# Kernel optimization log

Hardware: AMD Instinct MI355X
Metric: run time of the kernel (lower is better)

The kernel has to match this reference:

```python
import jax, jax.numpy as jnp
import numpy as np

B, N, P = 16, 128, 4096          # images, proposals/img, pairs/img
D_IN, D_HID = 1024, 512          # input_dim, hidden_dim
D_GEO, D_EMB = 128, 200          # geometry_feat_dim, embed_dim
N_OBJ, N_REL = 151, 51           # obj classes, rel classes (out_dim = 50)
OUT = N_REL - 1
LN_EPS = 1e-5


def _ln(x, g, b):
    mu = jnp.mean(x, axis=-1, keepdims=True)
    var = jnp.var(x, axis=-1, keepdims=True)
    return (x - mu) * jax.lax.rsqrt(var + LN_EPS) * g + b


def setup_inputs() -> dict:
    key = jax.random.key(0)
    ks = jax.random.split(key, 20)
    w = lambda k, shape: (jax.random.normal(k, shape, jnp.float32) * 0.02)
    return {
        'visual_feat': jax.random.normal(ks[0], (B * P, D_IN), jnp.float32),
        'box_info': jax.random.uniform(ks[1], (B, N, 9), jnp.float32),
        'pred_logits': jax.random.normal(ks[2], (B, N, N_OBJ), jnp.float32),
        'pair_idx': jax.random.randint(ks[3], (B, P, 2), 0, N, jnp.int32),
        'obj_sem_w': w(ks[4], (N_OBJ, D_EMB)),
        'pos_w1': w(ks[5], (9, D_GEO)), 'pos_b1': jnp.zeros((D_GEO,), jnp.float32),
        'pos_w2': w(ks[6], (D_GEO, D_GEO)), 'pos_b2': jnp.zeros((D_GEO,), jnp.float32),
        'vis_w': w(ks[7], (D_IN, D_HID)), 'vis_b': jnp.zeros((D_HID,), jnp.float32),
        'geo_w': w(ks[8], (2 * D_EMB + 2 * D_GEO, D_HID)), 'geo_b': jnp.zeros((D_HID,), jnp.float32),
        'fus_g': jnp.ones((2 * D_HID,), jnp.float32), 'fus_bt': jnp.zeros((2 * D_HID,), jnp.float32),
        'fus_w': w(ks[9], (2 * D_HID, D_HID)), 'fus_b': jnp.zeros((D_HID,), jnp.float32),
        'cls_g': jnp.ones((D_HID,), jnp.float32), 'cls_bt': jnp.zeros((D_HID,), jnp.float32),
        'cls_w': w(ks[10], (D_HID, OUT)), 'cls_b': jnp.zeros((OUT,), jnp.float32),
    }


def reference(visual_feat, box_info, pred_logits, pair_idx,
              obj_sem_w, pos_w1, pos_b1, pos_w2, pos_b2,
              vis_w, vis_b, geo_w, geo_b,
              fus_g, fus_bt, fus_w, fus_b,
              cls_g, cls_bt, cls_w, cls_b):
    # detach() in torch -> stop_gradient
    vf = jax.lax.stop_gradient(visual_feat)
    pl = jax.lax.stop_gradient(pred_logits)
    # vis_embed = Sequential(ReLU, Linear): [B*P, D_IN] -> [B, P, D_HID]
    vis = (jnp.maximum(vf, 0.0) @ vis_w + vis_b).reshape(B, P, D_HID)
    # obj_pos_embed = Linear, ReLU, Linear: [B, N, 9] -> [B, N, D_GEO]
    pos = jnp.maximum(box_info @ pos_w1 + pos_b1, 0.0) @ pos_w2 + pos_b2
    # semantic embed: softmax over obj classes @ embedding table -> [B, N, D_EMB]
    sem = jax.nn.softmax(pl, axis=-1) @ obj_sem_w
    bidx = jnp.arange(B)[:, None]
    s, o = pair_idx[..., 0], pair_idx[..., 1]
    # gather pair reps: [B, P, 2*(D_GEO+D_EMB)]
    rep = jnp.concatenate([pos[bidx, s], sem[bidx, s], pos[bidx, o], sem[bidx, o]], axis=-1)
    # proposal_box_feat_extract = Sequential(ReLU, Linear)
    geo = jnp.maximum(rep, 0.0) @ geo_w + geo_b
    # proposal_feat_fusion = Sequential(LayerNorm, ReLU, Linear)
    fused = jnp.concatenate([vis, geo], axis=-1)
    fused = jnp.maximum(_ln(fused, fus_g, fus_bt), 0.0) @ fus_w + fus_b
    # proposal_relness_cls_fc = Sequential(LayerNorm, ReLU, Linear)
    logits = jnp.maximum(_ln(fused, cls_g, cls_bt), 0.0) @ cls_w + cls_b  # [B, P, OUT]
    # predictor_type == 'single': scatter max sigmoid score into NxN matrix
    scores = jnp.max(jax.nn.sigmoid(logits), axis=-1)  # [B, P]
    rel_mat = jnp.zeros((B, N, N), logits.dtype).at[bidx, s, o].set(scores)
    return logits.reshape(B * P, OUT), rel_mat
```

## Files before the change

kernel.cpp:

```cpp
#include <hip/hip_runtime.h>
#include <cstdint>

#define B_    16
#define N_    128
#define P_    4096
#define M_    65536
#define DIN   1024
#define DHID  512
#define DGEO  128
#define DEMB  200
#define NODEF 328
#define NOBJ  151
#define OUTC  50
#define KGEO  656
#define KGEOP 672

typedef __attribute__((ext_vector_type(8))) short bf16x8;
typedef __attribute__((ext_vector_type(4))) float f32x4;

typedef __attribute__((address_space(3))) unsigned char lds_u8;
typedef __attribute__((address_space(1))) unsigned char glb_u8;

static __device__ __forceinline__ void async_copy16(const void* g, void* l) {
  __builtin_amdgcn_global_load_lds((const glb_u8*)g, (lds_u8*)l, 16, 0, 0);
}

static __device__ __forceinline__ unsigned short f2b(float f) {
  union { float f; unsigned u; } v; v.f = f;
  unsigned r = v.u + 0x7fffu + ((v.u >> 16) & 1u);
  return (unsigned short)(r >> 16);
}
static __device__ __forceinline__ float b2f(unsigned short b) {
  union { unsigned u; float f; } v; v.u = ((unsigned)b) << 16;
  return v.f;
}
static __device__ __forceinline__ unsigned pack2(float a, float b) {
  return (unsigned)f2b(a) | ((unsigned)f2b(b) << 16);
}
static __device__ __forceinline__ void unpack8(uint4 raw, float* x) {
  x[0] = b2f(raw.x & 0xffffu); x[1] = b2f(raw.x >> 16);
  x[2] = b2f(raw.y & 0xffffu); x[3] = b2f(raw.y >> 16);
  x[4] = b2f(raw.z & 0xffffu); x[5] = b2f(raw.z >> 16);
  x[6] = b2f(raw.w & 0xffffu); x[7] = b2f(raw.w >> 16);
}

#define ZN   131072
#define TV   (512 * 1024)
#define TG   (512 * KGEOP)
#define TF   (512 * 1024)
#define TC   (128 * 512)
#define PREP_TOT (ZN + TV + TG + TF + TC)
__global__ __launch_bounds__(256)
void prep_kernel(uint4* __restrict__ scat,
                 const float* __restrict__ vis_w, unsigned short* __restrict__ wT_vis,
                 const float* __restrict__ geo_w, unsigned short* __restrict__ wT_geo,
                 const float* __restrict__ fus_w, unsigned short* __restrict__ wT_fus,
                 const float* __restrict__ cls_w, unsigned short* __restrict__ wT_cls) {
  int idx = blockIdx.x * 256 + threadIdx.x;
  if (idx < ZN) { scat[idx] = make_uint4(0, 0, 0, 0); return; }
  idx -= ZN;
  if (idx < TV) {
    int n = idx >> 10, k = idx & 1023;
    wT_vis[idx] = f2b(vis_w[(size_t)k * 512 + n]);
    return;
  }
  idx -= TV;
  if (idx < TG) {
    int n = idx / KGEOP, k = idx - n * KGEOP;
    wT_geo[idx] = (k < KGEO) ? f2b(geo_w[(size_t)k * 512 + n]) : 0;
    return;
  }
  idx -= TG;
  if (idx < TF) {
    int n = idx >> 10, k = idx & 1023;
    wT_fus[idx] = f2b(fus_w[(size_t)k * 512 + n]);
    return;
  }
  idx -= TF;
  if (idx < TC) {
    int n = idx >> 9, k = idx & 511;
    wT_cls[idx] = (n < OUTC) ? f2b(cls_w[(size_t)k * OUTC + n]) : 0;
  }
}

__global__ __launch_bounds__(128)
void node_kernel(const float* __restrict__ box, const float* __restrict__ plog,
                 const float* __restrict__ semw,
                 const float* __restrict__ w1, const float* __restrict__ b1,
                 const float* __restrict__ w2, const float* __restrict__ b2,
                 unsigned short* __restrict__ nodeFb) {
  const int node = blockIdx.x;
  const int t = threadIdx.x;
  __shared__ float sBox[9];
  __shared__ float sH[128];
  __shared__ float sE[NOBJ];
  __shared__ float sRed[4];
  if (t < 9) sBox[t] = box[node * 9 + t];
  float l0 = (t < NOBJ) ? plog[node * NOBJ + t] : -1e30f;
  float l1 = (t + 128 < NOBJ) ? plog[node * NOBJ + t + 128] : -1e30f;
  __syncthreads();
  float h = b1[t];
#pragma unroll
  for (int i = 0; i < 9; i++) h = fmaf(sBox[i], w1[i * 128 + t], h);
  h = fmaxf(h, 0.f);
  sH[t] = h;
  float mx = fmaxf(l0, l1);
#pragma unroll
  for (int off = 32; off >= 1; off >>= 1) mx = fmaxf(mx, __shfl_xor(mx, off));
  if ((t & 63) == 0) sRed[t >> 6] = mx;
  __syncthreads();
  mx = fmaxf(sRed[0], sRed[1]);
  float e0 = (t < NOBJ) ? expf(l0 - mx) : 0.f;
  float e1 = (t + 128 < NOBJ) ? expf(l1 - mx) : 0.f;
  if (t < NOBJ) sE[t] = e0;
  if (t + 128 < NOBJ) sE[t + 128] = e1;
  float sm = e0 + e1;
#pragma unroll
  for (int off = 32; off >= 1; off >>= 1) sm += __shfl_xor(sm, off);
  if ((t & 63) == 0) sRed[2 + (t >> 6)] = sm;
  __syncthreads();
  const float inv = 1.f / (sRed[2] + sRed[3]);
  float pv = b2[t];
  for (int i = 0; i < 128; i++) pv = fmaf(sH[i], w2[i * 128 + t], pv);
  nodeFb[(size_t)node * NODEF + t] = f2b(fmaxf(pv, 0.f));
  float a0 = 0.f, a1 = 0.f;
  const int d1 = (t + 128 < DEMB) ? (t + 128) : 0;
  for (int i = 0; i < NOBJ; i++) {
    float e = sE[i];
    a0 = fmaf(e, semw[i * DEMB + t], a0);
    a1 = fmaf(e, semw[i * DEMB + d1], a1);
  }
  nodeFb[(size_t)node * NODEF + 128 + t] = f2b(fmaxf(a0 * inv, 0.f));
  if (t + 128 < DEMB) nodeFb[(size_t)node * NODEF + 128 + t + 128] = f2b(fmaxf(a1 * inv, 0.f));
}

template<int D>
__global__ __launch_bounds__(256)
void ln_relu_kernel(unsigned short* __restrict__ X,
                    const float* __restrict__ g, const float* __restrict__ bta) {
  constexpr int C = D / 64;
  const int lane = threadIdx.x & 63, wv = threadIdx.x >> 6;
  const size_t row = (size_t)blockIdx.x * 4 + wv;
  unsigned short* xp = X + row * D + lane * C;
  float x[C];
#pragma unroll
  for (int c = 0; c < C; c += 8) {
    uint4 raw = *(const uint4*)(xp + c);
    unpack8(raw, x + c);
  }
  float s = 0.f, s2 = 0.f;
#pragma unroll
  for (int q = 0; q < C; q++) { s += x[q]; s2 = fmaf(x[q], x[q], s2); }
#pragma unroll
  for (int off = 32; off >= 1; off >>= 1) { s += __shfl_xor(s, off); s2 += __shfl_xor(s2, off); }
  const float mu = s / D;
  const float rs = rsqrtf(s2 / D - mu * mu + 1e-5f);
  const float* gp = g + lane * C;
  const float* bp = bta + lane * C;
#pragma unroll
  for (int c = 0; c < C; c += 8) {
    float4 g0 = *(const float4*)(gp + c), g1 = *(const float4*)(gp + c + 4);
    float4 t0 = *(const float4*)(bp + c), t1 = *(const float4*)(bp + c + 4);
    float y0 = fmaxf(fmaf((x[c + 0] - mu) * rs, g0.x, t0.x), 0.f);
    float y1 = fmaxf(fmaf((x[c + 1] - mu) * rs, g0.y, t0.y), 0.f);
    float y2 = fmaxf(fmaf((x[c + 2] - mu) * rs, g0.z, t0.z), 0.f);
    float y3 = fmaxf(fmaf((x[c + 3] - mu) * rs, g0.w, t0.w), 0.f);
    float y4 = fmaxf(fmaf((x[c + 4] - mu) * rs, g1.x, t1.x), 0.f);
    float y5 = fmaxf(fmaf((x[c + 5] - mu) * rs, g1.y, t1.y), 0.f);
    float y6 = fmaxf(fmaf((x[c + 6] - mu) * rs, g1.z, t1.z), 0.f);
    float y7 = fmaxf(fmaf((x[c + 7] - mu) * rs, g1.w, t1.w), 0.f);
    uint4 u;
    u.x = pack2(y0, y1); u.y = pack2(y2, y3);
    u.z = pack2(y4, y5); u.w = pack2(y6, y7);
    *(uint4*)(xp + c) = u;
  }
}

template<int MODE>
__global__ __launch_bounds__(512, 4)
void gemmW(const void* __restrict__ Asrc, int ldaE,
           const unsigned short* __restrict__ Bt, int Ktot,
           const float* __restrict__ bias,
           unsigned short* __restrict__ C, int ldcE, int ccol0,
           const int* __restrict__ pidx,
           const unsigned short* __restrict__ nodeFb,
           const unsigned short* __restrict__ zsrc) {
  const int NS = Ktot >> 5;
  __shared__ __align__(16) unsigned char smem[8192 + 65536];
  const int tid = threadIdx.x, lane = tid & 63, w = tid >> 6;
  const int bm = blockIdx.x;

  const int ar = tid >> 3;
  const int ak = tid & 7;
  const int aswz = (ar & 3) ^ ((ar >> 2) & 3);
  unsigned char* aDst = smem + ar * 64 + (((ak >> 1) ^ aswz) << 4) + (ak & 1) * 8;

  const unsigned short* nbS = nullptr;
  const unsigned short* nbO = nullptr;
  const unsigned char* aG = nullptr;
  if (MODE == 2) {
    int pr = bm * 64 + ar;
    int2 so = *(const int2*)(pidx + 2 * pr);
    int b = pr >> 12;
    nbS = nodeFb + (size_t)((b << 7) + so.x) * NODEF;
    nbO = nodeFb + (size_t)((b << 7) + so.y) * NODEF;
  } else if (MODE == 1) {
    aG = (const unsigned char*)Asrc + (size_t)(bm * 64 + ar) * ldaE * 4 + ak * 16;
  } else {
    aG = (const unsigned char*)Asrc + (size_t)(bm * 64 + ar) * ldaE * 2 + ak * 8;
  }

  const int gsB = (lane & 3) ^ ((lane >> 2) & 3) ^ ((lane >> 4) & 3);
  int bOff[4];
#pragma unroll
  for (int i = 0; i < 4; i++) {
    int col = (w * 4 + i) * 16 + (lane >> 2);
    bOff[i] = col * Ktot * 2 + gsB * 16;
  }
  const unsigned char* bBase = (const unsigned char*)Bt;

  uint2 ra2[2]; uint4 ra4[2];
  auto issueA = [&](int s, int set) {
    if (MODE == 0) {
      ra2[set] = *(const uint2*)(aG + (size_t)s * 64);
    } else if (MODE == 1) {
      ra4[set] = *(const uint4*)(aG + (size_t)s * 128);
    } else {
      const int e0 = s * 32 + ak * 4;
      uintptr_t sel = (e0 < NODEF) ? (uintptr_t)(nbS + e0)
                    : (e0 < KGEO)  ? (uintptr_t)(nbO + (e0 - NODEF))
                                   : (uintptr_t)zsrc;
      ra2[set] = *(const uint2*)sel;
    }
  };
  auto issueB = [&](int s) {
    unsigned char* lb = smem + 8192 + (s & 1) * 32768 + w * 4096;
#pragma unroll
    for (int i = 0; i < 4; i++)
      async_copy16(bBase + (size_t)bOff[i] + (size_t)s * 64, lb + i * 1024);
  };
  auto writeA = [&](int s, int set) {
    uint2 d;
    if (MODE == 1) {
      float f0 = fmaxf(__uint_as_float(ra4[set].x), 0.f);
      float f1 = fmaxf(__uint_as_float(ra4[set].y), 0.f);
      float f2 = fmaxf(__uint_as_float(ra4[set].z), 0.f);
      float f3 = fmaxf(__uint_as_float(ra4[set].w), 0.f);
      d.x = pack2(f0, f1); d.y = pack2(f2, f3);
    } else d = ra2[set];
    *(uint2*)(aDst + (s & 1) * 4096) = d;
  };

  const int wm = w >> 2, wn = w & 3;
  const int frow = lane & 15;
  const int szf = (frow & 3) ^ ((frow >> 2) & 3);
  const int koff = (((lane >> 4) ^ szf) << 4);
  const int aRowB = (wm * 32 + frow) * 64;
  const int bColB = (wn * 128 + frow) * 64;

  f32x4 acc[2][8];
#pragma unroll
  for (int m = 0; m < 2; m++)
#pragma unroll
    for (int n = 0; n < 8; n++) acc[m][n] = (f32x4){0.f, 0.f, 0.f, 0.f};

  issueA(0, 0); issueB(0);
  issueA(1, 1); issueB(1);

#pragma unroll 1
  for (int s2 = 0; s2 < NS; s2 += 2) {
#pragma unroll
    for (int h = 0; h < 2; h++) {
      const int sc = s2 + h;
      if (sc >= NS) break;
      if (sc == NS - 1) asm volatile("s_waitcnt vmcnt(0)" ::: "memory");
      else              asm volatile("s_waitcnt vmcnt(5)" ::: "memory");
      __builtin_amdgcn_sched_barrier(0);
      writeA(sc, h);
      if (sc + 2 < NS) issueA(sc + 2, h);
      asm volatile("s_waitcnt lgkmcnt(0)" ::: "memory");
      __builtin_amdgcn_s_barrier();
      __builtin_amdgcn_sched_barrier(0);
      const unsigned char* ab = smem + (sc & 1) * 4096;
      const unsigned char* bb = smem + 8192 + (sc & 1) * 32768;
      bf16x8 af0 = *(const bf16x8*)(ab + aRowB + koff);
      bf16x8 af1 = *(const bf16x8*)(ab + aRowB + 16 * 64 + koff);
      __builtin_amdgcn_s_setprio(1);
#pragma unroll
      for (int n = 0; n < 8; n++) {
        bf16x8 bf = *(const bf16x8*)(bb + bColB + n * 16 * 64 + koff);
        acc[0][n] = __builtin_amdgcn_mfma_f32_16x16x32_bf16(af0, bf, acc[0][n], 0, 0, 0);
        acc[1][n] = __builtin_amdgcn_mfma_f32_16x16x32_bf16(af1, bf, acc[1][n], 0, 0, 0);
      }
      __builtin_amdgcn_s_setprio(0);
      __builtin_amdgcn_sched_barrier(0);
      __builtin_amdgcn_s_barrier();
      __builtin_amdgcn_sched_barrier(0);
      if (sc + 2 < NS) issueB(sc + 2);
    }
  }
  const int rb = bm * 64 + wm * 32 + ((lane >> 4) << 2);
  const int cb = wn * 128 + frow;
#pragma unroll
  for (int n = 0; n < 8; n++) {
    const int col = cb + n * 16;
    const float bv = bias[col];
#pragma unroll
    for (int m = 0; m < 2; m++)
#pragma unroll
      for (int i = 0; i < 4; i++) {
        const int row = rb + m * 16 + i;
        C[(size_t)row * ldcE + ccol0 + col] = f2b(acc[m][n][i] + bv);
      }
  }
}

__global__ __launch_bounds__(256)
void gemm_cls(const unsigned short* __restrict__ A, int lda,
              const unsigned short* __restrict__ Bt,
              const float* __restrict__ bias,
              float* __restrict__ C,
              int Ktot,
              const int* __restrict__ pidx,
              unsigned long long* __restrict__ scat) {
  __shared__ unsigned short ldsA[128 * 64];
  __shared__ unsigned short ldsB[128 * 64];
  const int tid = threadIdx.x;
  const int lane = tid & 63, wid = tid >> 6;
  const int cpx = gridDim.x >> 3;
  const int bm = (blockIdx.x & 7) * cpx + (blockIdx.x >> 3);

  const int srow = wid * 32 + (lane >> 3);
  const int skof = (lane & 7) * 8;
  const unsigned short* ag = A + (size_t)(bm * 128 + srow) * lda + skof;
  const unsigned short* bg = Bt + (size_t)srow * Ktot + skof;

  f32x4 acc[4][4];
#pragma unroll
  for (int m = 0; m < 4; m++)
#pragma unroll
    for (int n = 0; n < 4; n++) acc[m][n] = (f32x4){0.f, 0.f, 0.f, 0.f};

  const int wm = wid >> 1, wn = wid & 1;
  const int frow = lane & 15;
  const int kgrp = (lane >> 4) << 3;

  for (int kt = 0; kt < Ktot; kt += 64) {
#pragma unroll
    for (int i = 0; i < 4; i++) {
      async_copy16(ag + (size_t)i * 8 * lda + kt, &ldsA[wid * 2048 + i * 512]);
      async_copy16(bg + (size_t)i * 8 * Ktot + kt, &ldsB[wid * 2048 + i * 512]);
    }
    __syncthreads();
#pragma unroll
    for (int kk = 0; kk < 64; kk += 32) {
      bf16x8 af[4], bfr[4];
#pragma unroll
      for (int m = 0; m < 4; m++)
        af[m] = *(const bf16x8*)&ldsA[(wm * 64 + m * 16 + frow) * 64 + kk + kgrp];
#pragma unroll
      for (int n = 0; n < 4; n++)
        bfr[n] = *(const bf16x8*)&ldsB[(wn * 64 + n * 16 + frow) * 64 + kk + kgrp];
#pragma unroll
      for (int m = 0; m < 4; m++)
#pragma unroll
        for (int n = 0; n < 4; n++)
          acc[m][n] = __builtin_amdgcn_mfma_f32_16x16x32_bf16(af[m], bfr[n], acc[m][n], 0, 0, 0);
    }
    __syncthreads();
  }
  const int rb = bm * 128 + wm * 64 + ((lane >> 4) << 2);
#pragma unroll
  for (int n = 0; n < 4; n++) {
    const int col = wn * 64 + frow + n * 16;
    const float bv = (col < OUTC) ? bias[col] : 0.f;
#pragma unroll
    for (int m = 0; m < 4; m++)
#pragma unroll
      for (int i = 0; i < 4; i++) {
        const int row = rb + m * 16 + i;
        if (col < OUTC) C[(size_t)row * OUTC + col] = acc[m][n][i] + bv;
      }
  }
  if (wn == 0) {
#pragma unroll
    for (int m = 0; m < 4; m++)
#pragma unroll
      for (int i = 0; i < 4; i++) {
        float mx = -1e30f;
#pragma unroll
        for (int n = 0; n < 4; n++) {
          const int col = n * 16 + frow;
          float v = acc[m][n][i] + ((col < OUTC) ? bias[col] : 0.f);
          if (col < OUTC) mx = fmaxf(mx, v);
        }
        mx = fmaxf(mx, __shfl_xor(mx, 1));
        mx = fmaxf(mx, __shfl_xor(mx, 2));
        mx = fmaxf(mx, __shfl_xor(mx, 4));
        mx = fmaxf(mx, __shfl_xor(mx, 8));
        if (frow == 0) {
          const int row = rb + m * 16 + i;
          float sc = 1.f / (1.f + expf(-mx));
          int b = row >> 12, p = row & 4095;
          int s = pidx[2 * row], o = pidx[2 * row + 1];
          unsigned long long key = (((unsigned long long)(p + 1)) << 32) |
                                   (unsigned long long)__float_as_uint(sc);
          atomicMax(&scat[((size_t)(b * N_ + s) << 7) + o], key);
        }
      }
  }
}

__global__ void relmat_kernel(const unsigned long long* __restrict__ scat, float* __restrict__ out) {
  int i = blockIdx.x * blockDim.x + threadIdx.x;
  if (i >= B_ * N_ * N_) return;
  unsigned long long v = scat[i];
  out[i] = v ? __uint_as_float((unsigned)(v & 0xffffffffu)) : 0.f;
}

extern "C" void kernel_launch(void* const* d_in, const int* in_sizes, int n_in,
                              void* d_out, int out_size, void* d_ws, size_t ws_size,
                              hipStream_t stream) {
  const float* visual_feat = (const float*)d_in[0];
  const float* box_info    = (const float*)d_in[1];
  const float* pred_logits = (const float*)d_in[2];
  const int*   pair_idx    = (const int*)d_in[3];
  const float* obj_sem_w   = (const float*)d_in[4];
  const float* pos_w1 = (const float*)d_in[5];
  const float* pos_b1 = (const float*)d_in[6];
  const float* pos_w2 = (const float*)d_in[7];
  const float* pos_b2 = (const float*)d_in[8];
  const float* vis_w  = (const float*)d_in[9];
  const float* vis_b  = (const float*)d_in[10];
  const float* geo_w  = (const float*)d_in[11];
  const float* geo_b  = (const float*)d_in[12];
  const float* fus_g  = (const float*)d_in[13];
  const float* fus_bt = (const float*)d_in[14];
  const float* fus_w  = (const float*)d_in[15];
  const float* fus_b  = (const float*)d_in[16];
  const float* cls_g  = (const float*)d_in[17];
  const float* cls_bt = (const float*)d_in[18];
  const float* cls_w  = (const float*)d_in[19];
  const float* cls_b  = (const float*)d_in[20];

  char* ws = (char*)d_ws;
  size_t off = 0;
  auto alloc = [&](size_t bytes) { char* p = ws + off; off += (bytes + 255) & ~(size_t)255; return p; };
  unsigned short* fused  = (unsigned short*)alloc((size_t)M_ * 1024 * 2);
  unsigned short* fused2 = (unsigned short*)alloc((size_t)M_ * 512 * 2);
  unsigned short* nodeFb = (unsigned short*)alloc((size_t)B_ * N_ * NODEF * 2);
  unsigned short* wT_vis = (unsigned short*)alloc((size_t)512 * 1024 * 2);
  unsigned short* wT_geo = (unsigned short*)alloc((size_t)512 * KGEOP * 2);
  unsigned short* wT_fus = (unsigned short*)alloc((size_t)512 * 1024 * 2);
  unsigned short* wT_cls = (unsigned short*)alloc((size_t)128 * 512 * 2);
  unsigned long long* scat = (unsigned long long*)alloc((size_t)B_ * N_ * N_ * 8);

  float* out_logits = (float*)d_out;
  float* out_rel = out_logits + (size_t)M_ * OUTC;

  prep_kernel<<<dim3((PREP_TOT + 255) / 256), 256, 0, stream>>>(
      (uint4*)scat, vis_w, wT_vis, geo_w, wT_geo, fus_w, wT_fus, cls_w, wT_cls);
  node_kernel<<<dim3(B_ * N_), 128, 0, stream>>>(box_info, pred_logits, obj_sem_w,
                                                 pos_w1, pos_b1, pos_w2, pos_b2, nodeFb);
  gemmW<2><<<dim3(M_ / 64), 512, 0, stream>>>(nullptr, 0, wT_geo, KGEOP, geo_b,
                                              fused, 1024, 512,
                                              pair_idx, nodeFb, (const unsigned short*)scat);
  gemmW<1><<<dim3(M_ / 64), 512, 0, stream>>>(visual_feat, 1024, wT_vis, 1024, vis_b,
                                              fused, 1024, 0,
                                              nullptr, nullptr, nullptr);
  ln_relu_kernel<1024><<<dim3(M_ / 4), 256, 0, stream>>>(fused, fus_g, fus_bt);
  gemmW<0><<<dim3(M_ / 64), 512, 0, stream>>>(fused, 1024, wT_fus, 1024, fus_b,
                                              fused2, 512, 0,
                                              nullptr, nullptr, nullptr);
  ln_relu_kernel<512><<<dim3(M_ / 4), 256, 0, stream>>>(fused2, cls_g, cls_bt);
  gemm_cls<<<dim3(512), 256, 0, stream>>>(fused2, 512, wT_cls, cls_b,
                                          out_logits, 512, pair_idx, scat);
  relmat_kernel<<<dim3((B_ * N_ * N_) / 256), 256, 0, stream>>>(scat, out_rel);
}
```

Before: 464.7 us.

## Stage GEMM A tiles via async LDS copies with 4-deep pipeline; prepass relu-cast vis input

The GEMM kernel now loads its A operand with direct global-to-LDS async copies issued by half the waves into a 4-stage ring buffer, instead of loading through registers and writing LDS by hand. The LDS swizzle changes to match. Because the fp32 visual features cannot be relu'd and cast in flight anymore, a separate relu+bf16 cast kernel writes a bf16 copy into a reused workspace buffer before the visual GEMM. This is meant to deepen prefetch and cut register traffic and VALU work in the GEMM main loop. The cost is an extra full pass over the 256 MB fp32 input plus a 128 MB bf16 write, and more LDS per block.

```diff
diff --git a/kernel.cpp b/kernel.cpp
--- a/kernel.cpp
+++ b/kernel.cpp
@@ -134,6 +134,20 @@
   if (t + 128 < DEMB) nodeFb[(size_t)node * NODEF + 128 + t + 128] = f2b(fmaxf(a1 * inv, 0.f));
 }
 
+__global__ __launch_bounds__(256)
+void relu_cast_kernel(const float* __restrict__ in, unsigned short* __restrict__ out, int n8) {
+  for (int i = blockIdx.x * blockDim.x + threadIdx.x; i < n8; i += gridDim.x * blockDim.x) {
+    float4 v0 = ((const float4*)in)[2 * i];
+    float4 v1 = ((const float4*)in)[2 * i + 1];
+    uint4 u;
+    u.x = pack2(fmaxf(v0.x, 0.f), fmaxf(v0.y, 0.f));
+    u.y = pack2(fmaxf(v0.z, 0.f), fmaxf(v0.w, 0.f));
+    u.z = pack2(fmaxf(v1.x, 0.f), fmaxf(v1.y, 0.f));
+    u.w = pack2(fmaxf(v1.z, 0.f), fmaxf(v1.w, 0.f));
+    ((uint4*)out)[i] = u;
+  }
+}
+
 template<int D>
 __global__ __launch_bounds__(256)
 void ln_relu_kernel(unsigned short* __restrict__ X,
@@ -178,83 +192,69 @@
 
 template<int MODE>
 __global__ __launch_bounds__(512, 4)
-void gemmW(const void* __restrict__ Asrc, int ldaE,
-           const unsigned short* __restrict__ Bt, int Ktot,
-           const float* __restrict__ bias,
-           unsigned short* __restrict__ C, int ldcE, int ccol0,
-           const int* __restrict__ pidx,
-           const unsigned short* __restrict__ nodeFb,
-           const unsigned short* __restrict__ zsrc) {
+void gemmW2(const unsigned short* __restrict__ A, int ldaE,
+            const unsigned short* __restrict__ Bt, int Ktot,
+            const float* __restrict__ bias,
+            unsigned short* __restrict__ C, int ldcE, int ccol0,
+            const int* __restrict__ pidx,
+            const unsigned short* __restrict__ nodeFb,
+            const unsigned short* __restrict__ zsrc) {
   const int NS = Ktot >> 5;
-  __shared__ __align__(16) unsigned char smem[8192 + 65536];
+  __shared__ __align__(16) unsigned char smem[16384 + 65536];
   const int tid = threadIdx.x, lane = tid & 63, w = tid >> 6;
   const int bm = blockIdx.x;
 
-  const int ar = tid >> 3;
-  const int ak = tid & 7;
-  const int aswz = (ar & 3) ^ ((ar >> 2) & 3);
-  unsigned char* aDst = smem + ar * 64 + (((ak >> 1) ^ aswz) << 4) + (ak & 1) * 8;
-
+  const unsigned short* aS = nullptr;
   const unsigned short* nbS = nullptr;
   const unsigned short* nbO = nullptr;
-  const unsigned char* aG = nullptr;
-  if (MODE == 2) {
-    int pr = bm * 64 + ar;
-    int2 so = *(const int2*)(pidx + 2 * pr);
-    int b = pr >> 12;
-    nbS = nodeFb + (size_t)((b << 7) + so.x) * NODEF;
-    nbO = nodeFb + (size_t)((b << 7) + so.y) * NODEF;
-  } else if (MODE == 1) {
-    aG = (const unsigned char*)Asrc + (size_t)(bm * 64 + ar) * ldaE * 4 + ak * 16;
-  } else {
-    aG = (const unsigned char*)Asrc + (size_t)(bm * 64 + ar) * ldaE * 2 + ak * 8;
-  }
-
-  const int gsB = (lane & 3) ^ ((lane >> 2) & 3) ^ ((lane >> 4) & 3);
+  int aslot8 = 0;
+  if (w < 4) {
+    const int arow = w * 16 + (lane >> 2);
+    const int aslot = (lane & 3) ^ ((lane >> 3) & 3);
+    aslot8 = aslot * 8;
+    if (MODE == 0) {
+      aS = A + (size_t)(bm * 64 + arow) * ldaE + aslot8;
+    } else {
+      int pr = bm * 64 + arow;
+      int2 so = *(const int2*)(pidx + 2 * pr);
+      int b = pr >> 12;
+      nbS = nodeFb + (size_t)((b << 7) + so.x) * NODEF;
+      nbO = nodeFb + (size_t)((b << 7) + so.y) * NODEF;
+    }
+  }
+  auto stageA = [&](int s) {
+    if (w < 4) {
+      unsigned char* la = smem + (s & 3) * 4096 + w * 1024;
+      if (MODE == 0) {
+        async_copy16(aS + (size_t)s * 32, la);
+      } else {
+        const int e = s * 32 + aslot8;
+        uintptr_t sel = (e < NODEF) ? (uintptr_t)(nbS + e)
+                      : (e < KGEO)  ? (uintptr_t)(nbO + (e - NODEF))
+                                    : (uintptr_t)zsrc;
+        async_copy16((const void*)sel, la);
+      }
+    }
+  };
+
+  const unsigned char* bBase = (const unsigned char*)Bt;
+  const int gsB = (lane & 3) ^ ((lane >> 3) & 3);
   int bOff[4];
 #pragma unroll
   for (int i = 0; i < 4; i++) {
     int col = (w * 4 + i) * 16 + (lane >> 2);
     bOff[i] = col * Ktot * 2 + gsB * 16;
   }
-  const unsigned char* bBase = (const unsigned char*)Bt;
-
-  uint2 ra2[2]; uint4 ra4[2];
-  auto issueA = [&](int s, int set) {
-    if (MODE == 0) {
-      ra2[set] = *(const uint2*)(aG + (size_t)s * 64);
-    } else if (MODE == 1) {
-      ra4[set] = *(const uint4*)(aG + (size_t)s * 128);
-    } else {
-      const int e0 = s * 32 + ak * 4;
-      uintptr_t sel = (e0 < NODEF) ? (uintptr_t)(nbS + e0)
-                    : (e0 < KGEO)  ? (uintptr_t)(nbO + (e0 - NODEF))
-                                   : (uintptr_t)zsrc;
-      ra2[set] = *(const uint2*)sel;
-    }
-  };
-  auto issueB = [&](int s) {
-    unsigned char* lb = smem + 8192 + (s & 1) * 32768 + w * 4096;
+  auto stageB = [&](int s) {
+    unsigned char* lb = smem + 16384 + (s & 1) * 32768 + w * 4096;
 #pragma unroll
     for (int i = 0; i < 4; i++)
       async_copy16(bBase + (size_t)bOff[i] + (size_t)s * 64, lb + i * 1024);
   };
-  auto writeA = [&](int s, int set) {
-    uint2 d;
-    if (MODE == 1) {
-      float f0 = fmaxf(__uint_as_float(ra4[set].x), 0.f);
-      float f1 = fmaxf(__uint_as_float(ra4[set].y), 0.f);
-      float f2 = fmaxf(__uint_as_float(ra4[set].z), 0.f);
-      float f3 = fmaxf(__uint_as_float(ra4[set].w), 0.f);
-      d.x = pack2(f0, f1); d.y = pack2(f2, f3);
-    } else d = ra2[set];
-    *(uint2*)(aDst + (s & 1) * 4096) = d;
-  };
 
   const int wm = w >> 2, wn = w & 3;
   const int frow = lane & 15;
-  const int szf = (frow & 3) ^ ((frow >> 2) & 3);
-  const int koff = (((lane >> 4) ^ szf) << 4);
+  const int koff = (((lane >> 4) ^ ((frow >> 1) & 3)) << 4);
   const int aRowB = (wm * 32 + frow) * 64;
   const int bColB = (wn * 128 + frow) * 64;
 
@@ -264,40 +264,36 @@
 #pragma unroll
     for (int n = 0; n < 8; n++) acc[m][n] = (f32x4){0.f, 0.f, 0.f, 0.f};
 
-  issueA(0, 0); issueB(0);
-  issueA(1, 1); issueB(1);
+  stageA(0); stageA(1); stageA(2); stageA(3);
+  stageB(0); stageB(1);
 
 #pragma unroll 1
-  for (int s2 = 0; s2 < NS; s2 += 2) {
-#pragma unroll
-    for (int h = 0; h < 2; h++) {
-      const int sc = s2 + h;
-      if (sc >= NS) break;
-      if (sc == NS - 1) asm volatile("s_waitcnt vmcnt(0)" ::: "memory");
-      else              asm volatile("s_waitcnt vmcnt(5)" ::: "memory");
-      __builtin_amdgcn_sched_barrier(0);
-      writeA(sc, h);
-      if (sc + 2 < NS) issueA(sc + 2, h);
-      asm volatile("s_waitcnt lgkmcnt(0)" ::: "memory");
-      __builtin_amdgcn_s_barrier();
-      __builtin_amdgcn_sched_barrier(0);
-      const unsigned char* ab = smem + (sc & 1) * 4096;
-      const unsigned char* bb = smem + 8192 + (sc & 1) * 32768;
-      bf16x8 af0 = *(const bf16x8*)(ab + aRowB + koff);
-      bf16x8 af1 = *(const bf16x8*)(ab + aRowB + 16 * 64 + koff);
-      __builtin_amdgcn_s_setprio(1);
-#pragma unroll
-      for (int n = 0; n < 8; n++) {
-        bf16x8 bf = *(const bf16x8*)(bb + bColB + n * 16 * 64 + koff);
-        acc[0][n] = __builtin_amdgcn_mfma_f32_16x16x32_bf16(af0, bf, acc[0][n], 0, 0, 0);
-        acc[1][n] = __builtin_amdgcn_mfma_f32_16x16x32_bf16(af1, bf, acc[1][n], 0, 0, 0);
-      }
-      __builtin_amdgcn_s_setprio(0);
-      __builtin_amdgcn_sched_barrier(0);
-      __builtin_amdgcn_s_barrier();
-      __builtin_amdgcn_sched_barrier(0);
-      if (sc + 2 < NS) issueB(sc + 2);
+  for (int sc = 0; sc < NS; ++sc) {
+    if (sc == NS - 1)
+      asm volatile("s_waitcnt vmcnt(0)" ::: "memory");
+    else if (w >= 4 || sc == 0 || sc >= NS - 3)
+      asm volatile("s_waitcnt vmcnt(4)" ::: "memory");
+    else
+      asm volatile("s_waitcnt vmcnt(5)" ::: "memory");
+    __builtin_amdgcn_s_barrier();
+    __builtin_amdgcn_sched_barrier(0);
+    const unsigned char* ab = smem + (sc & 3) * 4096;
+    const unsigned char* bb = smem + 16384 + (sc & 1) * 32768;
+    bf16x8 af0 = *(const bf16x8*)(ab + aRowB + koff);
+    bf16x8 af1 = *(const bf16x8*)(ab + aRowB + 16 * 64 + koff);
+    __builtin_amdgcn_s_setprio(1);
+#pragma unroll
+    for (int n = 0; n < 8; n++) {
+      bf16x8 bf = *(const bf16x8*)(bb + bColB + n * 16 * 64 + koff);
+      acc[0][n] = __builtin_amdgcn_mfma_f32_16x16x32_bf16(af0, bf, acc[0][n], 0, 0, 0);
+      acc[1][n] = __builtin_amdgcn_mfma_f32_16x16x32_bf16(af1, bf, acc[1][n], 0, 0, 0);
     }
+    __builtin_amdgcn_s_setprio(0);
+    __builtin_amdgcn_sched_barrier(0);
+    __builtin_amdgcn_s_barrier();
+    __builtin_amdgcn_sched_barrier(0);
+    if (sc + 4 < NS) stageA(sc + 4);
+    if (sc + 2 < NS) stageB(sc + 2);
   }
   const int rb = bm * 64 + wm * 32 + ((lane >> 4) << 2);
   const int cb = wn * 128 + frow;
@@ -446,8 +442,8 @@
   char* ws = (char*)d_ws;
   size_t off = 0;
   auto alloc = [&](size_t bytes) { char* p = ws + off; off += (bytes + 255) & ~(size_t)255; return p; };
-  unsigned short* fused  = (unsigned short*)alloc((size_t)M_ * 1024 * 2);
-  unsigned short* fused2 = (unsigned short*)alloc((size_t)M_ * 512 * 2);
+  unsigned short* fused = (unsigned short*)alloc((size_t)M_ * 1024 * 2);
+  unsigned short* R1    = (unsigned short*)alloc((size_t)M_ * 1024 * 2);
   unsigned short* nodeFb = (unsigned short*)alloc((size_t)B_ * N_ * NODEF * 2);
   unsigned short* wT_vis = (unsigned short*)alloc((size_t)512 * 1024 * 2);
   unsigned short* wT_geo = (unsigned short*)alloc((size_t)512 * KGEOP * 2);
@@ -455,6 +451,9 @@
   unsigned short* wT_cls = (unsigned short*)alloc((size_t)128 * 512 * 2);
   unsigned long long* scat = (unsigned long long*)alloc((size_t)B_ * N_ * N_ * 8);
 
+  unsigned short* visA   = R1;
+  unsigned short* fused2 = R1;
+
   float* out_logits = (float*)d_out;
   float* out_rel = out_logits + (size_t)M_ * OUTC;
 
@@ -462,16 +461,17 @@
       (uint4*)scat, vis_w, wT_vis, geo_w, wT_geo, fus_w, wT_fus, cls_w, wT_cls);
   node_kernel<<<dim3(B_ * N_), 128, 0, stream>>>(box_info, pred_logits, obj_sem_w,
                                                  pos_w1, pos_b1, pos_w2, pos_b2, nodeFb);
-  gemmW<2><<<dim3(M_ / 64), 512, 0, stream>>>(nullptr, 0, wT_geo, KGEOP, geo_b,
-                                              fused, 1024, 512,
-                                              pair_idx, nodeFb, (const unsigned short*)scat);
-  gemmW<1><<<dim3(M_ / 64), 512, 0, stream>>>(visual_feat, 1024, wT_vis, 1024, vis_b,
-                                              fused, 1024, 0,
-                                              nullptr, nullptr, nullptr);
+  gemmW2<2><<<dim3(M_ / 64), 512, 0, stream>>>(nullptr, 0, wT_geo, KGEOP, geo_b,
+                                               fused, 1024, 512,
+                                               pair_idx, nodeFb, (const unsigned short*)scat);
+  relu_cast_kernel<<<dim3(2048), 256, 0, stream>>>(visual_feat, visA, M_ * 1024 / 8);
+  gemmW2<0><<<dim3(M_ / 64), 512, 0, stream>>>(visA, 1024, wT_vis, 1024, vis_b,
+                                               fused, 1024, 0,
+                                               nullptr, nullptr, nullptr);
   ln_relu_kernel<1024><<<dim3(M_ / 4), 256, 0, stream>>>(fused, fus_g, fus_bt);
-  gemmW<0><<<dim3(M_ / 64), 512, 0, stream>>>(fused, 1024, wT_fus, 1024, fus_b,
-                                              fused2, 512, 0,
-                                              nullptr, nullptr, nullptr);
+  gemmW2<0><<<dim3(M_ / 64), 512, 0, stream>>>(fused, 1024, wT_fus, 1024, fus_b,
+                                               fused2, 512, 0,
+                                               nullptr, nullptr, nullptr);
   ln_relu_kernel<512><<<dim3(M_ / 4), 256, 0, stream>>>(fused2, cls_g, cls_bt);
   gemm_cls<<<dim3(512), 256, 0, stream>>>(fused2, 512, wT_cls, cls_b,
                                           out_logits, 512, pair_idx, scat);
```

Result: slower. 506.1 us (+8.9%).
